# Kernel optimization log

Hardware: AMD Instinct MI355X
Metric: run time of the kernel (lower is better)

The kernel has to match this reference:

```python
import jax, jax.numpy as jnp
import numpy as np

VOCAB, EMBED, HIDDEN = 32000, 256, 512
B, S = 64, 64


def setup_inputs() -> dict:
    key = jax.random.key(0)
    ks = jax.random.split(key, 10)
    target_seq = jax.random.randint(ks[0], (B, S), 0, VOCAB)
    context = jax.random.normal(ks[1], (B, HIDDEN), dtype=jnp.float32)
    h = jax.random.normal(ks[2], (B, HIDDEN), dtype=jnp.float32)
    c = jax.random.normal(ks[3], (B, HIDDEN), dtype=jnp.float32)
    # parameters (torch default-ish init scale)
    emb_table = jax.random.normal(ks[4], (VOCAB, EMBED), dtype=jnp.float32)
    k_lstm = 1.0 / np.sqrt(HIDDEN)
    w_ih = jax.random.uniform(ks[5], (4 * HIDDEN, EMBED + HIDDEN), minval=-k_lstm, maxval=k_lstm, dtype=jnp.float32)
    w_hh = jax.random.uniform(ks[6], (4 * HIDDEN, HIDDEN), minval=-k_lstm, maxval=k_lstm, dtype=jnp.float32)
    b_ih = jax.random.uniform(ks[7], (4 * HIDDEN,), minval=-k_lstm, maxval=k_lstm, dtype=jnp.float32)
    b_hh = jnp.zeros((4 * HIDDEN,), dtype=jnp.float32)
    k_fc = 1.0 / np.sqrt(2 * HIDDEN)
    w_fc = jax.random.uniform(ks[8], (VOCAB, 2 * HIDDEN), minval=-k_fc, maxval=k_fc, dtype=jnp.float32)
    b_fc = jax.random.uniform(ks[9], (VOCAB,), minval=-k_fc, maxval=k_fc, dtype=jnp.float32)
    return dict(target_seq=target_seq, context=context, h=h, c=c,
                emb_table=emb_table, w_ih=w_ih, w_hh=w_hh, b_ih=b_ih, b_hh=b_hh,
                w_fc=w_fc, b_fc=b_fc)


def _decode(target_seq, context, h, c, emb_table, w_ih, w_hh, b_ih, b_hh, w_fc, b_fc):
    # teacher_forcing_ratio = 1.0 -> input at step t is target_seq[:, t]
    emb = emb_table[target_seq]                                    # [B,S,E]
    ctx_t = jnp.broadcast_to(context[:, None, :], (emb.shape[0], emb.shape[1], context.shape[1]))
    lstm_in = jnp.concatenate([emb, ctx_t], axis=-1)               # [B,S,E+H]
    # precompute input-to-hidden part of gates for all steps
    pre = jnp.einsum('bsf,gf->bsg', lstm_in, w_ih) + b_ih + b_hh   # [B,S,4H]
    H = h.shape[1]

    def step(carry, pre_t):
        h_t, c_t = carry
        gates = pre_t + h_t @ w_hh.T                               # [B,4H]
        i, f, g, o = jnp.split(gates, 4, axis=-1)
        i, f, o = jax.nn.sigmoid(i), jax.nn.sigmoid(f), jax.nn.sigmoid(o)
        g = jnp.tanh(g)
        c_n = f * c_t + i * g
        h_n = o * jnp.tanh(c_n)
        return (h_n, c_n), h_n

    _, hs = jax.lax.scan(step, (h, c), jnp.swapaxes(pre, 0, 1))    # hs: [S,B,H]
    hs = jnp.swapaxes(hs, 0, 1)                                    # [B,S,H]
    out_in = jnp.concatenate([hs, ctx_t], axis=-1)                 # [B,S,2H]
    logits = jnp.einsum('bsf,vf->bsv', out_in, w_fc) + b_fc        # [B,S,V]
    return logits


def reference(target_seq, context, h, c, emb_table, w_ih, w_hh, b_ih, b_hh, w_fc, b_fc):
    return _decode(target_seq, context, h, c, emb_table, w_ih, w_hh, b_ih, b_hh, w_fc, b_fc)
```

## Files before the change

### kernel.cpp

```cpp
#include <hip/hip_runtime.h>
#include <hip/hip_bf16.h>

#define VOCAB 32000
#define EMBED 256
#define HIDDEN 512
#define BB 64
#define SS 64
#define M_ROWS (BB * SS)
#define G4 (4 * HIDDEN)
#define NBLK 16
#define NTOT 256
#define NTILE_N (VOCAB / 256)
#define NITEM 1000

typedef __attribute__((ext_vector_type(8))) short short8v;
typedef __attribute__((ext_vector_type(4))) float float4v;
typedef __attribute__((ext_vector_type(4))) unsigned int uint4v;

__device__ __forceinline__ ushort f2bf(float f) {
    union { float f; unsigned u; } v; v.f = f;
    unsigned r = (v.u + 0x7FFFu + ((v.u >> 16) & 1u)) >> 16;
    return (ushort)r;
}

__device__ __forceinline__ float fast_tanh(float x) {
    float xc = fminf(fmaxf(x, -15.f), 15.f);
    float e = __expf(2.f * xc);
    return (e - 1.f) / (e + 1.f);
}

__device__ __forceinline__ void glds16(const ushort* g, ushort* l) {
    __builtin_amdgcn_global_load_lds(
        (const __attribute__((address_space(1))) unsigned int*)(const void*)g,
        (__attribute__((address_space(3))) unsigned int*)(void*)l, 16, 0, 0);
}

__global__ void k_conv_strided(const float* __restrict__ in, ushort* __restrict__ out,
                               int lg2cols, int instride, int n8) {
    int i = blockIdx.x * blockDim.x + threadIdx.x;
    int stride = gridDim.x * blockDim.x;
    int colmask = (1 << lg2cols) - 1;
    for (; i < n8; i += stride) {
        int i8 = i << 3;
        int row = i8 >> lg2cols, col = i8 & colmask;
        const float* src = in + (size_t)row * instride + col;
        float4 v0 = *(const float4*)src;
        float4 v1 = *(const float4*)(src + 4);
        short8v o;
        o[0] = (short)f2bf(v0.x); o[1] = (short)f2bf(v0.y);
        o[2] = (short)f2bf(v0.z); o[3] = (short)f2bf(v0.w);
        o[4] = (short)f2bf(v1.x); o[5] = (short)f2bf(v1.y);
        o[6] = (short)f2bf(v1.z); o[7] = (short)f2bf(v1.w);
        *(short8v*)(out + i8) = o;
    }
}

__global__ void k_build_emb(const int* __restrict__ tseq, const float* __restrict__ emb,
                            ushort* __restrict__ embbf) {
    int rid = blockIdx.x * 8 + (threadIdx.x >> 5);
    int c0 = (threadIdx.x & 31) * 8;
    int tok = tseq[rid];
    const float* src = emb + (size_t)tok * EMBED + c0;
    float4 v0 = *(const float4*)src;
    float4 v1 = *(const float4*)(src + 4);
    short8v o;
    o[0] = (short)f2bf(v0.x); o[1] = (short)f2bf(v0.y);
    o[2] = (short)f2bf(v0.z); o[3] = (short)f2bf(v0.w);
    o[4] = (short)f2bf(v1.x); o[5] = (short)f2bf(v1.y);
    o[6] = (short)f2bf(v1.z); o[7] = (short)f2bf(v1.w);
    *(short8v*)(embbf + (size_t)rid * EMBED + c0) = o;
}

__global__ void k_prep_small(const float* __restrict__ b_ih, const float* __restrict__ b_hh,
                             float* __restrict__ bias_pre,
                             const float* __restrict__ h0, ushort* __restrict__ hbufA,
                             const float* __restrict__ ctx, ushort* __restrict__ ctx_bf,
                             unsigned* __restrict__ ctrl) {
    int i = blockIdx.x * blockDim.x + threadIdx.x;
    if (i < 1024) ctrl[i] = 0;
    if (i < G4) bias_pre[i] = b_ih[i] + b_hh[i];
    if (i < BB * HIDDEN) {
        hbufA[i] = f2bf(h0[i]);
        ctx_bf[i] = f2bf(ctx[i]);
    }
}

__global__ __launch_bounds__(256) void k_gemm_smallM(
    const ushort* __restrict__ Abf, const float* __restrict__ Wf, int wstride,
    const float* __restrict__ bias, float* __restrict__ Cout, int N) {
    int t = threadIdx.x;
    int wv = t >> 6, lane = t & 63, lr = lane & 15, kg = lane >> 4;
    int bcol = blockIdx.x * 128;

    float4v acc[4][2];
#pragma unroll
    for (int m = 0; m < 4; m++)
#pragma unroll
        for (int n = 0; n < 2; n++) acc[m][n] = (float4v){0.f, 0.f, 0.f, 0.f};

#pragma unroll 4
    for (int ks = 0; ks < 16; ks++) {
        short8v a[4];
#pragma unroll
        for (int m = 0; m < 4; m++)
            a[m] = *(const short8v*)(Abf + (size_t)(m * 16 + lr) * 512 + ks * 32 + kg * 8);
        short8v w[2];
#pragma unroll
        for (int n = 0; n < 2; n++) {
            const float* src = Wf + (size_t)(bcol + wv * 32 + n * 16 + lr) * wstride + ks * 32 + kg * 8;
            float4 v0 = *(const float4*)src;
            float4 v1 = *(const float4*)(src + 4);
            short8v w8;
            w8[0] = (short)f2bf(v0.x); w8[1] = (short)f2bf(v0.y);
            w8[2] = (short)f2bf(v0.z); w8[3] = (short)f2bf(v0.w);
            w8[4] = (short)f2bf(v1.x); w8[5] = (short)f2bf(v1.y);
            w8[6] = (short)f2bf(v1.z); w8[7] = (short)f2bf(v1.w);
            w[n] = w8;
        }
#pragma unroll
        for (int m = 0; m < 4; m++)
#pragma unroll
            for (int n = 0; n < 2; n++)
                acc[m][n] = __builtin_amdgcn_mfma_f32_16x16x32_bf16(a[m], w[n], acc[m][n], 0, 0, 0);
    }

#pragma unroll
    for (int n = 0; n < 2; n++) {
        int col = bcol + wv * 32 + n * 16 + lr;
        float bv = bias[col];
#pragma unroll
        for (int m = 0; m < 4; m++) {
            int row = m * 16 + kg * 4;
#pragma unroll
            for (int j = 0; j < 4; j++)
                Cout[(size_t)(row + j) * N + col] = acc[m][n][j] + bv;
        }
    }
}

__global__ __launch_bounds__(512) void k_gemm_bf16(
    const ushort* __restrict__ A, const ushort* __restrict__ W,
    const float* __restrict__ rowbias, float* __restrict__ C,
    int M, int N, int K) {
    __shared__ ushort As[256 * 32];
    __shared__ ushort Ws[256 * 32];
    int t = threadIdx.x;

    int gx = N >> 8, gy = M >> 8;
    int nwg = gx * gy;
    int q = nwg >> 3, r = nwg & 7;
    int xcd = blockIdx.x & 7, idx = blockIdx.x >> 3;
    int wg = (xcd < r) ? xcd * (q + 1) + idx : r * (q + 1) + (xcd - r) * q + idx;
    const int SG = 4;
    int grp = wg / (gx * SG);
    int rem = wg % (gx * SG);
    int bx = rem / SG;
    int by = grp * SG + rem % SG;
    int brow = by * 256, bcol = bx * 256;

    int wave = t >> 6, lane = t & 63;
    int wr = wave >> 2, wc = wave & 3;
    int lr = lane & 15, kg = lane >> 4;

    float4v acc[8][4];
#pragma unroll
    for (int m = 0; m < 8; m++)
#pragma unroll
        for (int n = 0; n < 4; n++) acc[m][n] = (float4v){0.f, 0.f, 0.f, 0.f};

    int srow = t >> 2;
    int scol = (((t & 3) ^ (srow & 3))) * 8;
    const ushort* AgA = A + (size_t)(brow + srow) * K + scol;
    const ushort* AgB = A + (size_t)(brow + 128 + srow) * K + scol;
    const ushort* WgA = W + (size_t)(bcol + srow) * K + scol;
    const ushort* WgB = W + (size_t)(bcol + 128 + srow) * K + scol;
    ushort* ldsA0 = &As[(wave * 16) * 32];
    ushort* ldsA1 = &As[(128 + wave * 16) * 32];
    ushort* ldsW0 = &Ws[(wave * 16) * 32];
    ushort* ldsW1 = &Ws[(128 + wave * 16) * 32];

    for (int bk = 0; bk < K; bk += 32) {
        glds16(AgA + bk, ldsA0);
        glds16(AgB + bk, ldsA1);
        glds16(WgA + bk, ldsW0);
        glds16(WgB + bk, ldsW1);
        __syncthreads();
        short8v a[8], w[4];
#pragma unroll
        for (int m = 0; m < 8; m++) {
            int row = wr * 128 + m * 16 + lr;
            a[m] = *(const short8v*)&As[row * 32 + (kg ^ (row & 3)) * 8];
        }
#pragma unroll
        for (int n = 0; n < 4; n++) {
            int row = wc * 64 + n * 16 + lr;
            w[n] = *(const short8v*)&Ws[row * 32 + (kg ^ (row & 3)) * 8];
        }
#pragma unroll
        for (int m = 0; m < 8; m++)
#pragma unroll
            for (int n = 0; n < 4; n++)
                acc[m][n] = __builtin_amdgcn_mfma_f32_16x16x32_bf16(a[m], w[n], acc[m][n], 0, 0, 0);
        __syncthreads();
    }

#pragma unroll
    for (int n = 0; n < 4; n++) {
        int col = bcol + wc * 64 + n * 16 + lr;
#pragma unroll
        for (int m = 0; m < 8; m++) {
            int row = brow + wr * 128 + m * 16 + kg * 4;
            float bv = rowbias[(size_t)(row >> 6) * N + col];
            float4v v = acc[m][n];
#pragma unroll
            for (int j = 0; j < 4; j++)
                C[(size_t)(row + j) * N + col] = v[j] + bv;
        }
    }
}

__global__ __launch_bounds__(512) void k_mega(
    const float* __restrict__ pre, const float* __restrict__ w_hh,
    const float* __restrict__ c0,
    ushort* __restrict__ hbufA,
    ushort* __restrict__ out_in, unsigned* __restrict__ ctrl,
    const ushort* __restrict__ Wfc, const float* __restrict__ ctxdot,
    float* __restrict__ Cout) {
    __shared__ __align__(16) char smem[147456];
    __shared__ int s_tile;
    unsigned* flags = ctrl;
    unsigned* queue = ctrl + 512;
    int t = threadIdx.x;
    int bid = blockIdx.x;
    int wave = t >> 6, lane = t & 63, lr = lane & 15, kg = lane >> 4;

    if (bid < NBLK) {
        ushort* h_lds = (ushort*)smem;
        float* G2 = (float*)(smem + 65536);
        char* hl = (char*)h_lds;
        int p = bid;
        int w = wave;
        int mh = w >> 2, cw2 = w & 3;

        short8v wfrag[2][16];
#pragma unroll
        for (int ci = 0; ci < 2; ci++) {
            const float* wrow = w_hh + (size_t)(cw2 * HIDDEN + p * 32 + ci * 16 + lr) * HIDDEN;
#pragma unroll
            for (int ks = 0; ks < 16; ks++) {
                const float* src = wrow + ks * 32 + kg * 8;
                short8v w8;
#pragma unroll
                for (int e = 0; e < 8; e++) w8[e] = (short)f2bf(src[e]);
                wfrag[ci][ks] = w8;
            }
        }

        int b = t >> 3, jj0 = (t & 7) * 4, jg0 = p * 32 + jj0;
        float4v c_reg = *(const float4v*)(c0 + (size_t)b * HIDDEN + jg0);
        float4v pv[4];
#pragma unroll
        for (int qg = 0; qg < 4; qg++)
            pv[qg] = *(const float4v*)(pre + (size_t)(b * SS) * G4 + qg * HIDDEN + jg0);

        for (int s = 0; s < SS; s++) {
            if (s > 0) {
                const unsigned* fp = flags + (lane & 15) * 16;
                unsigned fv;
                do {
                    fv = __hip_atomic_load(fp, __ATOMIC_RELAXED, __HIP_MEMORY_SCOPE_AGENT);
                } while (__all((int)(fv >= (unsigned)s)) == 0);
            }

            {
                const ushort* hb = (s == 0) ? hbufA
                                            : out_in + (size_t)(s - 1) * BB * HIDDEN;
                uint4v vb[8];
#pragma unroll
                for (int i = 0; i < 8; i++) {
                    int rr = w * 8 + i;
                    const void* src = hb + (size_t)rr * HIDDEN + lane * 8;
                    asm volatile("global_load_dwordx4 %0, %1, off sc0 sc1"
                                 : "=&v"(vb[i]) : "v"(src));
                }
                asm volatile("s_waitcnt vmcnt(0)" ::: "memory");
#pragma unroll
                for (int i = 0; i < 8; i++) {
                    int rr = w * 8 + i;
                    int off = (rr * 1024 + lane * 16) ^ ((rr & 7) << 4);
                    *(uint4v*)(hl + off) = vb[i];
                }
            }
            __syncthreads();

            float4v acc[2][2];
#pragma unroll
            for (int mi = 0; mi < 2; mi++)
#pragma unroll
                for (int ci = 0; ci < 2; ci++) acc[mi][ci] = (float4v){0.f, 0.f, 0.f, 0.f};
#pragma unroll
            for (int ks = 0; ks < 16; ks++) {
                short8v a[2];
#pragma unroll
                for (int mi = 0; mi < 2; mi++) {
                    int row = mh * 32 + mi * 16 + lr;
                    int off = (row * 1024 + ks * 64 + kg * 16) ^ ((row & 7) << 4);
                    a[mi] = *(const short8v*)(hl + off);
                }
#pragma unroll
                for (int mi = 0; mi < 2; mi++)
#pragma unroll
                    for (int ci = 0; ci < 2; ci++)
                        acc[mi][ci] = __builtin_amdgcn_mfma_f32_16x16x32_bf16(a[mi], wfrag[ci][ks], acc[mi][ci], 0, 0, 0);
            }
#pragma unroll
            for (int mi = 0; mi < 2; mi++)
#pragma unroll
                for (int ci = 0; ci < 2; ci++)
#pragma unroll
                    for (int rr = 0; rr < 4; rr++)
                        G2[(mh * 32 + mi * 16 + kg * 4 + rr) * 132 + cw2 * 32 + ci * 16 + lr] = acc[mi][ci][rr];
            __syncthreads();

            {
                float4v gq[4];
#pragma unroll
                for (int qg = 0; qg < 4; qg++) gq[qg] = *(const float4v*)&G2[b * 132 + qg * 32 + jj0];
                unsigned long long hv8 = 0;
#pragma unroll
                for (int e = 0; e < 4; e++) {
                    float xi = gq[0][e] + pv[0][e];
                    float xf = gq[1][e] + pv[1][e];
                    float xg = gq[2][e] + pv[2][e];
                    float xo = gq[3][e] + pv[3][e];
                    float ig = 1.f / (1.f + __expf(-xi));
                    float fg = 1.f / (1.f + __expf(-xf));
                    float gg = fast_tanh(xg);
                    float og = 1.f / (1.f + __expf(-xo));
                    float cn = fg * c_reg[e] + ig * gg;
                    float hv = og * fast_tanh(cn);
                    c_reg[e] = cn;
                    hv8 |= (unsigned long long)f2bf(hv) << (16 * e);
                }
                __hip_atomic_store((unsigned long long*)(out_in + (size_t)(s * BB + b) * HIDDEN + jg0), hv8,
                                   __ATOMIC_RELAXED, __HIP_MEMORY_SCOPE_AGENT);
                if (s + 1 < SS) {
#pragma unroll
                    for (int qg = 0; qg < 4; qg++)
                        pv[qg] = *(const float4v*)(pre + (size_t)(b * SS + s + 1) * G4 + qg * HIDDEN + jg0);
                }
            }

            __syncthreads();
            if (t == 0)
                __hip_atomic_store(flags + p * 16, (unsigned)(s + 1),
                                   __ATOMIC_RELEASE, __HIP_MEMORY_SCOPE_AGENT);
        }
    } else {
        ushort* As = (ushort*)smem;
        ushort* Ws = (ushort*)(smem + 131072);
        char* al = (char*)As;
        int srow = t >> 2;
        int scolW = ((t & 3) ^ (srow & 3)) * 8;
        ushort* ldsW0 = Ws + (wave * 16) * 32;
        ushort* ldsW1 = Ws + (128 + wave * 16) * 32;
        int wr = wave >> 2, wc = wave & 3;
        int last_hm = -1, last_gated = -1;

        for (;;) {
            __syncthreads();
            if (t == 0)
                s_tile = (int)__hip_atomic_fetch_add(queue, 1u, __ATOMIC_RELAXED, __HIP_MEMORY_SCOPE_AGENT);
            __syncthreads();
            int item = s_tile;
            if (item >= NITEM) break;
            int hm, nt0, cnt;
            if (item < 750) { hm = item / 25; nt0 = (item % 25) * 5; cnt = 5; }
            else { int j = item - 750; hm = 30 + j / 125; nt0 = j % 125; cnt = 1; }

            int need = 2 * hm + 2;
            if (need > last_gated) {
                if (wave == 0) {
                    const unsigned* fp = flags + (lane & 15) * 16;
                    for (;;) {
                        unsigned fv = __hip_atomic_load(fp, __ATOMIC_RELAXED, __HIP_MEMORY_SCOPE_AGENT);
                        if (__all((int)(fv >= (unsigned)need))) break;
                        asm volatile("s_sleep 64");
                    }
                }
                __syncthreads();
                last_gated = need;
            }

            if (hm != last_hm) {
                const ushort* Ab = out_in + (size_t)hm * 128 * HIDDEN;
#pragma unroll
                for (int half = 0; half < 2; half++) {
                    uint4v vb[8];
#pragma unroll
                    for (int i = 0; i < 8; i++) {
                        int rr = wave * 16 + half * 8 + i;
                        const void* src = Ab + (size_t)rr * HIDDEN + lane * 8;
                        asm volatile("global_load_dwordx4 %0, %1, off sc0 sc1"
                                     : "=&v"(vb[i]) : "v"(src));
                    }
                    asm volatile("s_waitcnt vmcnt(0)" ::: "memory");
#pragma unroll
                    for (int i = 0; i < 8; i++) {
                        int rr = wave * 16 + half * 8 + i;
                        int off = (rr * 1024 + lane * 16) ^ ((rr & 7) << 4);
                        *(uint4v*)(al + off) = vb[i];
                    }
                }
                __syncthreads();
                last_hm = hm;
            }

            for (int q5 = 0; q5 < cnt; q5++) {
                int nt = nt0 + q5;
                int bcol = nt * 256;

                float4v acc[4][4];
#pragma unroll
                for (int m = 0; m < 4; m++)
#pragma unroll
                    for (int n = 0; n < 4; n++) acc[m][n] = (float4v){0.f, 0.f, 0.f, 0.f};

                const ushort* WgA = Wfc + (size_t)(bcol + srow) * HIDDEN + scolW;
                const ushort* WgB = WgA + (size_t)128 * HIDDEN;

                for (int ks = 0; ks < 16; ks++) {
                    glds16(WgA + ks * 32, ldsW0);
                    glds16(WgB + ks * 32, ldsW1);
                    __syncthreads();
                    short8v a[4], w[4];
#pragma unroll
                    for (int m = 0; m < 4; m++) {
                        int row = wr * 64 + m * 16 + lr;
                        int off = (row * 1024 + ks * 64 + kg * 16) ^ ((row & 7) << 4);
                        a[m] = *(const short8v*)(al + off);
                    }
#pragma unroll
                    for (int n = 0; n < 4; n++) {
                        int wrow = wc * 64 + n * 16 + lr;
                        w[n] = *(const short8v*)&Ws[wrow * 32 + (kg ^ (wrow & 3)) * 8];
                    }
#pragma unroll
                    for (int m = 0; m < 4; m++)
#pragma unroll
                        for (int n = 0; n < 4; n++)
                            acc[m][n] = __builtin_amdgcn_mfma_f32_16x16x32_bf16(a[m], w[n], acc[m][n], 0, 0, 0);
                    __syncthreads();
                }

#pragma unroll
                for (int n = 0; n < 4; n++) {
                    int col = bcol + wc * 64 + n * 16 + lr;
#pragma unroll
                    for (int m = 0; m < 4; m++) {
                        int rbase = wr * 64 + m * 16 + kg * 4;
#pragma unroll
                        for (int j = 0; j < 4; j++) {
                            int rl = rbase + j;
                            int bb = rl & 63;
                            int ss = hm * 2 + (rl >> 6);
                            float val = acc[m][n][j] + ctxdot[(size_t)bb * VOCAB + col];
                            __builtin_nontemporal_store(val, &Cout[(size_t)(bb * 64 + ss) * VOCAB + col]);
                        }
                    }
                }
            }
        }
    }
}

extern "C" void kernel_launch(void* const* d_in, const int* in_sizes, int n_in,
                              void* d_out, int out_size, void* d_ws, size_t ws_size,
                              hipStream_t stream) {
    const int*   tseq = (const int*)d_in[0];
    const float* ctx  = (const float*)d_in[1];
    const float* h0   = (const float*)d_in[2];
    const float* c0   = (const float*)d_in[3];
    const float* emb  = (const float*)d_in[4];
    const float* w_ih = (const float*)d_in[5];
    const float* w_hh = (const float*)d_in[6];
    const float* b_ih = (const float*)d_in[7];
    const float* b_hh = (const float*)d_in[8];
    const float* w_fc = (const float*)d_in[9];
    const float* b_fc = (const float*)d_in[10];
    float* out = (float*)d_out;

    char* wsb = (char*)d_ws;
    size_t off = 0;
    auto alloc = [&](size_t bytes) -> void* {
        void* ptr = wsb + off;
        off = (off + bytes + 255) & ~(size_t)255;
        return ptr;
    };
    ushort* emb_bf    = (ushort*)alloc((size_t)M_ROWS * EMBED * 2);
    ushort* w_ih_ebf  = (ushort*)alloc((size_t)G4 * EMBED * 2);
    ushort* w_fc_hbf  = (ushort*)alloc((size_t)VOCAB * HIDDEN * 2);
    ushort* out_in    = (ushort*)alloc((size_t)M_ROWS * HIDDEN * 2);
    float*  pre       = (float*)alloc((size_t)M_ROWS * G4 * 4);
    float*  prectx    = (float*)alloc((size_t)BB * G4 * 4);
    float*  ctxdot    = (float*)alloc((size_t)BB * VOCAB * 4);
    ushort* ctx_bf    = (ushort*)alloc((size_t)BB * HIDDEN * 2);
    ushort* hbufA     = (ushort*)alloc((size_t)BB * HIDDEN * 2);
    float*  bias_pre  = (float*)alloc((size_t)G4 * 4);
    unsigned* ctrl    = (unsigned*)alloc(4096);

    k_conv_strided<<<256, 256, 0, stream>>>(w_ih, w_ih_ebf, 8, 768, G4 * EMBED / 8);
    k_conv_strided<<<2048, 256, 0, stream>>>(w_fc, w_fc_hbf, 9, 1024, VOCAB * HIDDEN / 8);
    k_build_emb<<<M_ROWS / 8, 256, 0, stream>>>(tseq, emb, emb_bf);
    k_prep_small<<<128, 256, 0, stream>>>(b_ih, b_hh, bias_pre, h0, hbufA, ctx, ctx_bf, ctrl);

    k_gemm_smallM<<<G4 / 128, 256, 0, stream>>>(ctx_bf, w_ih + 256, 768, bias_pre, prectx, G4);
    k_gemm_smallM<<<VOCAB / 128, 256, 0, stream>>>(ctx_bf, w_fc + 512, 1024, b_fc, ctxdot, VOCAB);

    k_gemm_bf16<<<dim3((G4 / 256) * (M_ROWS / 256)), 512, 0, stream>>>(
        emb_bf, w_ih_ebf, prectx, pre, M_ROWS, G4, EMBED);

    void* args[] = {(void*)&pre, (void*)&w_hh, (void*)&c0,
                    (void*)&hbufA, (void*)&out_in, (void*)&ctrl,
                    (void*)&w_fc_hbf, (void*)&ctxdot, (void*)&out};
    hipLaunchCooperativeKernel((void*)k_mega, dim3(NTOT), dim3(512), args, 0, stream);
}
```

Before: 649.9 us.

## Move w_fc conversion and context-logit GEMM into mega kernel worker queue

```diff
diff --git a/kernel.cpp b/kernel.cpp
--- a/kernel.cpp
+++ b/kernel.cpp
@@ -11,7 +11,9 @@
 #define NBLK 16
 #define NTOT 256
 #define NTILE_N (VOCAB / 256)
-#define NITEM 1000
+#define NP1_CONV 250
+#define NP1 375
+#define NITEM_TOT (NP1 + 1000)
 
 typedef __attribute__((ext_vector_type(8))) short short8v;
 typedef __attribute__((ext_vector_type(4))) float float4v;
@@ -224,12 +226,15 @@
     const float* __restrict__ c0,
     ushort* __restrict__ hbufA,
     ushort* __restrict__ out_in, unsigned* __restrict__ ctrl,
-    const ushort* __restrict__ Wfc, const float* __restrict__ ctxdot,
+    const float* __restrict__ w_fc, const float* __restrict__ b_fc,
+    ushort* __restrict__ Wfc, float* __restrict__ ctxdot,
+    const ushort* __restrict__ ctx_bf,
     float* __restrict__ Cout) {
     __shared__ __align__(16) char smem[147456];
     __shared__ int s_tile;
     unsigned* flags = ctrl;
     unsigned* queue = ctrl + 512;
+    unsigned* p1cnt = ctrl + 600;
     int t = threadIdx.x;
     int bid = blockIdx.x;
     int wave = t >> 6, lane = t & 63, lr = lane & 15, kg = lane >> 4;
@@ -366,6 +371,7 @@
         ushort* ldsW1 = Ws + (128 + wave * 16) * 32;
         int wr = wave >> 2, wc = wave & 3;
         int last_hm = -1, last_gated = -1;
+        bool p1_waited = false;
 
         for (;;) {
             __syncthreads();
@@ -373,10 +379,103 @@
                 s_tile = (int)__hip_atomic_fetch_add(queue, 1u, __ATOMIC_RELAXED, __HIP_MEMORY_SCOPE_AGENT);
             __syncthreads();
             int item = s_tile;
-            if (item >= NITEM) break;
+            if (item >= NITEM_TOT) break;
+
+            if (item < NP1_CONV) {
+                int r0 = item * 128;
+#pragma unroll
+                for (int k = 0; k < 16; k++) {
+                    int u = t + k * 512;
+                    int r = r0 + (u >> 6), c8 = (u & 63) * 8;
+                    const float* src = w_fc + (size_t)r * 1024 + c8;
+                    float4 v0 = *(const float4*)src;
+                    float4 v1 = *(const float4*)(src + 4);
+                    uint4v o;
+                    o[0] = (unsigned)f2bf(v0.x) | ((unsigned)f2bf(v0.y) << 16);
+                    o[1] = (unsigned)f2bf(v0.z) | ((unsigned)f2bf(v0.w) << 16);
+                    o[2] = (unsigned)f2bf(v1.x) | ((unsigned)f2bf(v1.y) << 16);
+                    o[3] = (unsigned)f2bf(v1.z) | ((unsigned)f2bf(v1.w) << 16);
+                    const void* dst = Wfc + (size_t)r * 512 + c8;
+                    asm volatile("global_store_dwordx4 %0, %1, off sc0 sc1"
+                                 :: "v"(dst), "v"(o) : "memory");
+                }
+                asm volatile("s_waitcnt vmcnt(0)" ::: "memory");
+                __syncthreads();
+                if (t == 0)
+                    __hip_atomic_fetch_add(p1cnt, 1u, __ATOMIC_RELAXED, __HIP_MEMORY_SCOPE_AGENT);
+                continue;
+            }
+            if (item < NP1) {
+                int bcol = (item - NP1_CONV) * 256;
+                float4v acc[4][2];
+#pragma unroll
+                for (int m = 0; m < 4; m++)
+#pragma unroll
+                    for (int n = 0; n < 2; n++) acc[m][n] = (float4v){0.f, 0.f, 0.f, 0.f};
+#pragma unroll 4
+                for (int ks = 0; ks < 16; ks++) {
+                    short8v a[4];
+#pragma unroll
+                    for (int m = 0; m < 4; m++)
+                        a[m] = *(const short8v*)(ctx_bf + (size_t)(m * 16 + lr) * 512 + ks * 32 + kg * 8);
+                    short8v w[2];
+#pragma unroll
+                    for (int n = 0; n < 2; n++) {
+                        const float* src = w_fc + (size_t)(bcol + wave * 32 + n * 16 + lr) * 1024 + 512 + ks * 32 + kg * 8;
+                        float4 v0 = *(const float4*)src;
+                        float4 v1 = *(const float4*)(src + 4);
+                        short8v w8;
+                        w8[0] = (short)f2bf(v0.x); w8[1] = (short)f2bf(v0.y);
+                        w8[2] = (short)f2bf(v0.z); w8[3] = (short)f2bf(v0.w);
+                        w8[4] = (short)f2bf(v1.x); w8[5] = (short)f2bf(v1.y);
+                        w8[6] = (short)f2bf(v1.z); w8[7] = (short)f2bf(v1.w);
+                        w[n] = w8;
+                    }
+#pragma unroll
+                    for (int m = 0; m < 4; m++)
+#pragma unroll
+                        for (int n = 0; n < 2; n++)
+                            acc[m][n] = __builtin_amdgcn_mfma_f32_16x16x32_bf16(a[m], w[n], acc[m][n], 0, 0, 0);
+                }
+#pragma unroll
+                for (int n = 0; n < 2; n++) {
+                    int col = bcol + wave * 32 + n * 16 + lr;
+                    float bv = b_fc[col];
+#pragma unroll
+                    for (int m = 0; m < 4; m++) {
+                        int row = m * 16 + kg * 4;
+#pragma unroll
+                        for (int j = 0; j < 4; j++) {
+                            float val = acc[m][n][j] + bv;
+                            const void* dst = ctxdot + (size_t)(row + j) * VOCAB + col;
+                            asm volatile("global_store_dword %0, %1, off sc0 sc1"
+                                         :: "v"(dst), "v"(val) : "memory");
+                        }
+                    }
+                }
+                asm volatile("s_waitcnt vmcnt(0)" ::: "memory");
+                __syncthreads();
+                if (t == 0)
+                    __hip_atomic_fetch_add(p1cnt, 1u, __ATOMIC_RELAXED, __HIP_MEMORY_SCOPE_AGENT);
+                continue;
+            }
+
+            if (!p1_waited) {
+                if (wave == 0) {
+                    for (;;) {
+                        unsigned v = __hip_atomic_load(p1cnt, __ATOMIC_RELAXED, __HIP_MEMORY_SCOPE_AGENT);
+                        if (v >= (unsigned)NP1) break;
+                        asm volatile("s_sleep 64");
+                    }
+                }
+                __syncthreads();
+                p1_waited = true;
+            }
+
+            int li = item - NP1;
             int hm, nt0, cnt;
-            if (item < 750) { hm = item / 25; nt0 = (item % 25) * 5; cnt = 5; }
-            else { int j = item - 750; hm = 30 + j / 125; nt0 = j % 125; cnt = 1; }
+            if (li < 750) { hm = li / 25; nt0 = (li % 25) * 5; cnt = 5; }
+            else { int j = li - 750; hm = 30 + j / 125; nt0 = j % 125; cnt = 1; }
 
             int need = 2 * hm + 2;
             if (need > last_gated) {
@@ -510,18 +609,15 @@
     unsigned* ctrl    = (unsigned*)alloc(4096);
 
     k_conv_strided<<<256, 256, 0, stream>>>(w_ih, w_ih_ebf, 8, 768, G4 * EMBED / 8);
-    k_conv_strided<<<2048, 256, 0, stream>>>(w_fc, w_fc_hbf, 9, 1024, VOCAB * HIDDEN / 8);
     k_build_emb<<<M_ROWS / 8, 256, 0, stream>>>(tseq, emb, emb_bf);
     k_prep_small<<<128, 256, 0, stream>>>(b_ih, b_hh, bias_pre, h0, hbufA, ctx, ctx_bf, ctrl);
-
     k_gemm_smallM<<<G4 / 128, 256, 0, stream>>>(ctx_bf, w_ih + 256, 768, bias_pre, prectx, G4);
-    k_gemm_smallM<<<VOCAB / 128, 256, 0, stream>>>(ctx_bf, w_fc + 512, 1024, b_fc, ctxdot, VOCAB);
-
     k_gemm_bf16<<<dim3((G4 / 256) * (M_ROWS / 256)), 512, 0, stream>>>(
         emb_bf, w_ih_ebf, prectx, pre, M_ROWS, G4, EMBED);
 
     void* args[] = {(void*)&pre, (void*)&w_hh, (void*)&c0,
                     (void*)&hbufA, (void*)&out_in, (void*)&ctrl,
-                    (void*)&w_fc_hbf, (void*)&ctxdot, (void*)&out};
+                    (void*)&w_fc, (void*)&b_fc, (void*)&w_fc_hbf, (void*)&ctxdot,
+                    (void*)&ctx_bf, (void*)&out};
     hipLaunchCooperativeKernel((void*)k_mega, dim3(NTOT), dim3(512), args, 0, stream);
 }
```

Measured after the change: 654.7 us. Within noise of the previous version (+0.7%).
